# Kernel optimization log

Measured on AMD Instinct MI355X. Metric: run time of the kernel, lower is better.

## Reference

```python
import jax, jax.numpy as jnp
import numpy as np

C = 512
GROUPS = 8
EPS = 1e-5


def setup_inputs() -> dict:
    key = jax.random.key(0)
    ks = jax.random.split(key, 7)
    B, H, W = 16, 32, 32
    x = jax.random.normal(ks[0], (B, C, H, W), dtype=jnp.float32)
    # GroupNorm affine params
    gn_scale = jnp.ones((C,), jnp.float32)
    gn_bias = jnp.zeros((C,), jnp.float32)
    # 1x1 convs == channel matmuls
    s_qkv = 1.0 / np.sqrt(C)
    qkv_w = jax.random.uniform(ks[1], (3 * C, C), jnp.float32, -s_qkv, s_qkv)
    qkv_b = jax.random.uniform(ks[2], (3 * C,), jnp.float32, -s_qkv, s_qkv)
    proj_w = jax.random.uniform(ks[3], (C, C), jnp.float32, -s_qkv, s_qkv)
    proj_b = jax.random.uniform(ks[4], (C,), jnp.float32, -s_qkv, s_qkv)
    return {"x": x, "gn_scale": gn_scale, "gn_bias": gn_bias,
            "qkv_w": qkv_w, "qkv_b": qkv_b, "proj_w": proj_w, "proj_b": proj_b}


def _group_norm(x, scale, bias):
    B, c, H, W = x.shape
    xg = x.reshape(B, GROUPS, c // GROUPS, H, W)
    mean = xg.mean(axis=(2, 3, 4), keepdims=True)
    var = xg.var(axis=(2, 3, 4), keepdims=True)
    xn = ((xg - mean) * jax.lax.rsqrt(var + EPS)).reshape(B, c, H, W)
    return xn * scale[None, :, None, None] + bias[None, :, None, None]


def reference(x, gn_scale, gn_bias, qkv_w, qkv_b, proj_w, proj_b):
    B, c, H, W = x.shape
    N = H * W
    h = _group_norm(x, gn_scale, gn_bias)            # [B,C,H,W]
    hf = h.reshape(B, c, N)                          # flatten spatial
    qkv = jnp.einsum('oc,bcn->bon', qkv_w, hf) + qkv_b[None, :, None]  # [B,3C,N]
    q, k, v = jnp.split(qkv, 3, axis=1)              # each [B,C,N]
    attn = jnp.einsum('bci,bcj->bij', q, k) * (c ** -0.5)  # [B,N,N]
    attn = jax.nn.softmax(attn, axis=2)
    out = jnp.einsum('bij,bcj->bci', attn, v)        # [B,C,N]
    out = jnp.einsum('oc,bcn->bon', proj_w, out) + proj_b[None, :, None]
    return out.reshape(B, c, H, W) + x
```

## Files before the change

kernel.cpp:

```cpp
#include <hip/hip_runtime.h>

typedef __bf16 bf16x8 __attribute__((ext_vector_type(8)));
typedef float f32x4 __attribute__((ext_vector_type(4)));
typedef unsigned short u16;

__device__ __forceinline__ u16 f2bf(float f) {
  unsigned u = __float_as_uint(f);
  u += 0x7fffu + ((u >> 16) & 1u);
  return (u16)(u >> 16);
}
__device__ __forceinline__ float bf2f(u16 h) {
  return __uint_as_float(((unsigned)h) << 16);
}

#define GLOAD_LDS(g, l)                                              \
  __builtin_amdgcn_global_load_lds(                                  \
      (const __attribute__((address_space(1))) void*)(g),            \
      (__attribute__((address_space(3))) void*)(l), 16, 0, 0)

template <int K>
__device__ __forceinline__ void gemm_core_s(const u16* __restrict__ Ab,
                                            const u16* __restrict__ Bb,
                                            f32x4 acc[4][4]) {
  __shared__ __align__(16) u16 As[2][8192], Bs[2][8192];
  const int tid = threadIdx.x;
  const int wave = tid >> 6, lane = tid & 63;
  const int sr = tid >> 3;
  const int sc = ((tid ^ sr) & 7) << 3;
  const u16* ag = Ab + (size_t)sr * K + sc;
  const u16* bg = Bb + (size_t)sr * K + sc;
  const int ldst = tid * 8;
  const int wr = (wave >> 1) << 6, wc = (wave & 1) << 6;
  const int lrow = lane & 15, klane = lane >> 4;
  const int rx = lrow & 7;
  const int ao = (wr + lrow) * 64 + ((klane ^ rx) << 3);
  const int bo = (wc + lrow) * 64 + ((klane ^ rx) << 3);

  const u16 *a_cur = As[0] + ldst, *a_nxt = As[1] + ldst;
  const u16 *b_cur = Bs[0] + ldst, *b_nxt = Bs[1] + ldst;
  const u16 *ar = As[0], *br = Bs[0];
  const u16 *an = As[1], *bn = Bs[1];

#pragma unroll
  for (int r = 0; r < 4; r++) GLOAD_LDS(ag + (size_t)(r * 32) * K, a_cur + r * 2048);
#pragma unroll
  for (int r = 0; r < 4; r++) GLOAD_LDS(bg + (size_t)(r * 32) * K, b_cur + r * 2048);
  __syncthreads();

  for (int k = 64; k < K; k += 64) {
#pragma unroll
    for (int r = 0; r < 4; r++) GLOAD_LDS(ag + (size_t)(r * 32) * K + k, a_nxt + r * 2048);
#pragma unroll
    for (int r = 0; r < 4; r++) GLOAD_LDS(bg + (size_t)(r * 32) * K + k, b_nxt + r * 2048);
#pragma unroll
    for (int half = 0; half < 2; half++) {
      const int xo = half << 5;
      bf16x8 a[4], b[4];
#pragma unroll
      for (int i = 0; i < 4; i++) a[i] = *(const bf16x8*)(ar + ((ao ^ xo) + (i << 10)));
#pragma unroll
      for (int i = 0; i < 4; i++) b[i] = *(const bf16x8*)(br + ((bo ^ xo) + (i << 10)));
#pragma unroll
      for (int mi = 0; mi < 4; mi++)
#pragma unroll
        for (int ni = 0; ni < 4; ni++)
          acc[mi][ni] = __builtin_amdgcn_mfma_f32_16x16x32_bf16(a[mi], b[ni], acc[mi][ni], 0, 0, 0);
    }
    __syncthreads();
    const u16* t;
    t = a_cur; a_cur = a_nxt; a_nxt = t;
    t = b_cur; b_cur = b_nxt; b_nxt = t;
    t = ar; ar = an; an = t;
    t = br; br = bn; bn = t;
  }
#pragma unroll
  for (int half = 0; half < 2; half++) {
    const int xo = half << 5;
    bf16x8 a[4], b[4];
#pragma unroll
    for (int i = 0; i < 4; i++) a[i] = *(const bf16x8*)(ar + ((ao ^ xo) + (i << 10)));
#pragma unroll
    for (int i = 0; i < 4; i++) b[i] = *(const bf16x8*)(br + ((bo ^ xo) + (i << 10)));
#pragma unroll
    for (int mi = 0; mi < 4; mi++)
#pragma unroll
      for (int ni = 0; ni < 4; ni++)
        acc[mi][ni] = __builtin_amdgcn_mfma_f32_16x16x32_bf16(a[mi], b[ni], acc[mi][ni], 0, 0, 0);
  }
}

#define ACC_INIT                                     \
  f32x4 acc[4][4];                                   \
  {                                                  \
    const f32x4 _z = {0.f, 0.f, 0.f, 0.f};           \
    _Pragma("unroll")                                \
    for (int _i = 0; _i < 4; _i++)                   \
      _Pragma("unroll")                              \
      for (int _j = 0; _j < 4; _j++) acc[_i][_j] = _z; \
  }

#define EPI_SETUP                                                            \
  const int tid = threadIdx.x;                                               \
  const int wave = tid >> 6;                                                 \
  const int lane = tid & 63;                                                 \
  const int mb = (blockIdx.y << 7) + ((wave >> 1) << 6) + (((lane >> 4) & 3) << 2); \
  const int nb = (blockIdx.x << 7) + ((wave & 1) << 6) + (lane & 15);

__global__ void __launch_bounds__(256) k_convw(const float* __restrict__ qw,
                                               const float* __restrict__ pw,
                                               u16* __restrict__ wq, u16* __restrict__ wp) {
  const int t = blockIdx.x * 256 + threadIdx.x;
  for (int i = t; i < 786432; i += 262144) wq[i] = f2bf(qw[i]);
  wp[t] = f2bf(pw[t]);
}

__global__ void __launch_bounds__(256) k_gn1(const float* __restrict__ x,
                                             float* __restrict__ part) {
  const int blk = blockIdx.x;
  const float4* src = (const float4*)(x + ((size_t)(blk >> 2) * 64 + (blk & 3) * 16) * 1024);
  float s1 = 0.f, s2 = 0.f;
  for (int i = threadIdx.x; i < 4096; i += 256) {
    float4 v = src[i];
    s1 += v.x + v.y + v.z + v.w;
    s2 += v.x * v.x + v.y * v.y + v.z * v.z + v.w * v.w;
  }
#pragma unroll
  for (int off = 32; off; off >>= 1) { s1 += __shfl_xor(s1, off); s2 += __shfl_xor(s2, off); }
  __shared__ float red[8];
  const int wave = threadIdx.x >> 6, lane = threadIdx.x & 63;
  if (lane == 0) { red[wave] = s1; red[4 + wave] = s2; }
  __syncthreads();
  if (threadIdx.x == 0) {
    part[blk * 2]     = red[0] + red[1] + red[2] + red[3];
    part[blk * 2 + 1] = red[4] + red[5] + red[6] + red[7];
  }
}

__global__ void __launch_bounds__(128) k_gn1b(const float* __restrict__ part,
                                              float* __restrict__ stats) {
  const int g = threadIdx.x;
  const float s1 = part[g * 8 + 0] + part[g * 8 + 2] + part[g * 8 + 4] + part[g * 8 + 6];
  const float s2 = part[g * 8 + 1] + part[g * 8 + 3] + part[g * 8 + 5] + part[g * 8 + 7];
  const float mean = s1 * (1.f / 65536.f);
  const float var = s2 * (1.f / 65536.f) - mean * mean;
  stats[g * 2]     = mean;
  stats[g * 2 + 1] = rsqrtf(var + 1e-5f);
}

__global__ void __launch_bounds__(256) k_gn2(const float* __restrict__ x,
                                             const float* __restrict__ gsc,
                                             const float* __restrict__ gbi,
                                             const float* __restrict__ stats,
                                             u16* __restrict__ h) {
  const int chunk = blockIdx.x & 7, g = (blockIdx.x >> 3) & 7, b = blockIdx.x >> 6;
  const int bg = b * 8 + g;
  const float mean = stats[bg * 2], rstd = stats[bg * 2 + 1];
  const float* xb = x + ((size_t)b * 512 + g * 64) * 1024;
  const int tid = threadIdx.x, wave = tid >> 6, lane = tid & 63;
  __shared__ u16 tile[64][66];
#pragma unroll
  for (int half = 0; half < 2; half++) {
    const int n0 = chunk * 128 + half * 64;
    if (half) __syncthreads();
#pragma unroll
    for (int r = 0; r < 16; r++) {
      const int cl = (r << 2) + wave;
      const int ch = (g << 6) + cl;
      float v = xb[(size_t)cl * 1024 + n0 + lane];
      tile[lane][cl] = f2bf((v - mean) * rstd * gsc[ch] + gbi[ch]);
    }
    __syncthreads();
#pragma unroll
    for (int r = 0; r < 16; r++) {
      const int nl = (r << 2) + wave;
      h[((size_t)b * 1024 + n0 + nl) * 512 + (g << 6) + lane] = tile[nl][lane];
    }
  }
}

__global__ void __launch_bounds__(256) k_qkv(const u16* __restrict__ W,
                                             const u16* __restrict__ h,
                                             const float* __restrict__ bias,
                                             u16* __restrict__ qt, u16* __restrict__ kt,
                                             u16* __restrict__ vv) {
  const int b = blockIdx.z;
  ACC_INIT
  gemm_core_s<512>(W + ((size_t)blockIdx.y << 7) * 512,
                   h + ((size_t)b << 19) + (((size_t)blockIdx.x << 7) * 512), acc);
  EPI_SETUP
  const int sel = blockIdx.y >> 2;
  const float scale = 0.044194173824159216f;
  if (sel < 2) {
    u16* dst = sel ? kt : qt;
    const float sc = sel ? 1.f : scale;
    const int obase = mb - sel * 512;
#pragma unroll
    for (int mi = 0; mi < 4; mi++) {
      const int o = mb + mi * 16;
#pragma unroll
      for (int ni = 0; ni < 4; ni++) {
        const int n = nb + ni * 16;
        ushort4 pk;
        pk.x = f2bf((acc[mi][ni][0] + bias[o + 0]) * sc);
        pk.y = f2bf((acc[mi][ni][1] + bias[o + 1]) * sc);
        pk.z = f2bf((acc[mi][ni][2] + bias[o + 2]) * sc);
        pk.w = f2bf((acc[mi][ni][3] + bias[o + 3]) * sc);
        *(ushort4*)(dst + ((size_t)b * 1024 + n) * 512 + (obase + mi * 16)) = pk;
      }
    }
  } else {
#pragma unroll
    for (int mi = 0; mi < 4; mi++) {
      const int o = mb + mi * 16;
#pragma unroll
      for (int ni = 0; ni < 4; ni++) {
        const int n = nb + ni * 16;
#pragma unroll
        for (int r = 0; r < 4; r++) {
          float val = acc[mi][ni][r] + bias[o + r];
          vv[((size_t)b * 512 + (o - 1024 + r)) * 1024 + n] = f2bf(val);
        }
      }
    }
  }
}

__global__ void __launch_bounds__(256) k_sgemm(const u16* __restrict__ qt,
                                               const u16* __restrict__ kt,
                                               u16* __restrict__ S) {
  const int b = blockIdx.z;
  ACC_INIT
  gemm_core_s<512>(qt + ((size_t)b << 19) + ((size_t)blockIdx.y << 7) * 512,
                   kt + ((size_t)b << 19) + ((size_t)blockIdx.x << 7) * 512, acc);
  EPI_SETUP
  const size_t base = (size_t)b << 20;
#pragma unroll
  for (int mi = 0; mi < 4; mi++)
#pragma unroll
    for (int ni = 0; ni < 4; ni++) {
      const int j = nb + ni * 16;
#pragma unroll
      for (int r = 0; r < 4; r++)
        S[base + (size_t)(mb + mi * 16 + r) * 1024 + j] = f2bf(acc[mi][ni][r]);
    }
}

__global__ void __launch_bounds__(256) k_softmax(u16* __restrict__ S) {
  const size_t base = (((size_t)blockIdx.y << 10) + blockIdx.x) << 10;
  const int tid = threadIdx.x;
  const int wave = tid >> 6, lane = tid & 63;
  ushort4 raw = *(const ushort4*)(S + base + tid * 4);
  float v0 = bf2f(raw.x), v1 = bf2f(raw.y), v2 = bf2f(raw.z), v3 = bf2f(raw.w);
  float m = fmaxf(fmaxf(v0, v1), fmaxf(v2, v3));
#pragma unroll
  for (int off = 32; off; off >>= 1) m = fmaxf(m, __shfl_xor(m, off));
  __shared__ float s1[4], s2[4];
  if (lane == 0) s1[wave] = m;
  __syncthreads();
  m = fmaxf(fmaxf(s1[0], s1[1]), fmaxf(s1[2], s1[3]));
  v0 = __expf(v0 - m); v1 = __expf(v1 - m); v2 = __expf(v2 - m); v3 = __expf(v3 - m);
  float s = v0 + v1 + v2 + v3;
#pragma unroll
  for (int off = 32; off; off >>= 1) s += __shfl_xor(s, off);
  if (lane == 0) s2[wave] = s;
  __syncthreads();
  s = s2[0] + s2[1] + s2[2] + s2[3];
  const float inv = 1.0f / s;
  raw.x = f2bf(v0 * inv); raw.y = f2bf(v1 * inv);
  raw.z = f2bf(v2 * inv); raw.w = f2bf(v3 * inv);
  *(ushort4*)(S + base + tid * 4) = raw;
}

__global__ void __launch_bounds__(256) k_ogemm(const u16* __restrict__ vv,
                                               const u16* __restrict__ P,
                                               u16* __restrict__ ot) {
  const int b = blockIdx.z;
  ACC_INIT
  gemm_core_s<1024>(vv + ((size_t)b << 19) + ((size_t)blockIdx.y << 7) * 1024,
                    P + ((size_t)b << 20) + ((size_t)blockIdx.x << 7) * 1024, acc);
  EPI_SETUP
#pragma unroll
  for (int mi = 0; mi < 4; mi++) {
    const int c = mb + mi * 16;
#pragma unroll
    for (int ni = 0; ni < 4; ni++) {
      const int i = nb + ni * 16;
      ushort4 pk;
      pk.x = f2bf(acc[mi][ni][0]);
      pk.y = f2bf(acc[mi][ni][1]);
      pk.z = f2bf(acc[mi][ni][2]);
      pk.w = f2bf(acc[mi][ni][3]);
      *(ushort4*)(ot + ((size_t)b << 19) + (size_t)i * 512 + c) = pk;
    }
  }
}

__global__ void __launch_bounds__(256) k_proj(const u16* __restrict__ W,
                                              const u16* __restrict__ ot,
                                              const float* __restrict__ pb,
                                              const float* __restrict__ x,
                                              float* __restrict__ out) {
  const int b = blockIdx.z;
  ACC_INIT
  gemm_core_s<512>(W + ((size_t)blockIdx.y << 7) * 512,
                   ot + ((size_t)b << 19) + ((size_t)blockIdx.x << 7) * 512, acc);
  EPI_SETUP
#pragma unroll
  for (int mi = 0; mi < 4; mi++) {
    const int o = mb + mi * 16;
#pragma unroll
    for (int ni = 0; ni < 4; ni++) {
      const int n = nb + ni * 16;
      const size_t base = ((size_t)b * 512 + o) * 1024 + n;
#pragma unroll
      for (int r = 0; r < 4; r++)
        out[base + (size_t)r * 1024] = acc[mi][ni][r] + pb[o + r] + x[base + (size_t)r * 1024];
    }
  }
}

extern "C" void kernel_launch(void* const* d_in, const int* in_sizes, int n_in,
                              void* d_out, int out_size, void* d_ws, size_t ws_size,
                              hipStream_t stream) {
  const float* x     = (const float*)d_in[0];
  const float* gsc   = (const float*)d_in[1];
  const float* gbi   = (const float*)d_in[2];
  const float* qkvw  = (const float*)d_in[3];
  const float* qkvb  = (const float*)d_in[4];
  const float* projw = (const float*)d_in[5];
  const float* projb = (const float*)d_in[6];
  float* out = (float*)d_out;

  char* ws = (char*)d_ws;
  u16* wq = (u16*)(ws);
  u16* wp = (u16*)(ws + 1572864);
  u16* h  = (u16*)(ws + 2097152);
  u16* qt = (u16*)(ws + 18874368);
  u16* kt = (u16*)(ws + 35651584);
  u16* vv = (u16*)(ws + 52428864);
  u16* S  = (u16*)(ws + 69206080);
  u16* ot = h;
  float* part  = (float*)(ws + 69206080);
  float* stats = (float*)(ws + 69206080 + 8192);

  k_convw<<<1024, 256, 0, stream>>>(qkvw, projw, wq, wp);
  k_gn1<<<512, 256, 0, stream>>>(x, part);
  k_gn1b<<<1, 128, 0, stream>>>(part, stats);
  k_gn2<<<1024, 256, 0, stream>>>(x, gsc, gbi, stats, h);
  k_qkv<<<dim3(8, 12, 16), 256, 0, stream>>>(wq, h, qkvb, qt, kt, vv);
  k_sgemm<<<dim3(8, 8, 16), 256, 0, stream>>>(qt, kt, S);
  k_softmax<<<dim3(1024, 16), 256, 0, stream>>>(S);
  k_ogemm<<<dim3(8, 4, 16), 256, 0, stream>>>(vv, S, ot);
  k_proj<<<dim3(8, 4, 16), 256, 0, stream>>>(wp, ot, projb, x, out);
}
```

Baseline: 250.6 us.

## Swizzle GEMM blocks across XCDs and fuse small GroupNorm/weight-convert kernels

Adds an XCD-aware block index remap to all four GEMM kernels, so that consecutive logical tiles (the same batch and neighbouring tiles) land on the same XCD and share its L2. It also folds the weight bf16 conversion into the GroupNorm statistics kernel and moves the tiny stats-finalize kernel into k_gn2, which removes two launches. The cost is extra integer division in each GEMM block and more work per block in k_gn1.

```diff
diff --git a/kernel.cpp b/kernel.cpp
--- a/kernel.cpp
+++ b/kernel.cpp
@@ -11,6 +11,17 @@
 }
 __device__ __forceinline__ float bf2f(u16 h) {
   return __uint_as_float(((unsigned)h) << 16);
+}
+
+__device__ __forceinline__ int3 xcd_swz(int gx, int gy, int gz) {
+  const int D = blockIdx.x + gx * (blockIdx.y + gy * blockIdx.z);
+  const int cpx = (gx * gy * gz) >> 3;
+  const int L = (D & 7) * cpx + (D >> 3);
+  int3 r;
+  r.x = L % gx;
+  r.y = (L / gx) % gy;
+  r.z = L / (gx * gy);
+  return r;
 }
 
 #define GLOAD_LDS(g, l)                                              \
@@ -99,23 +110,19 @@
       for (int _j = 0; _j < 4; _j++) acc[_i][_j] = _z; \
   }
 
-#define EPI_SETUP                                                            \
+#define EPI_SETUP(BX, BY)                                                    \
   const int tid = threadIdx.x;                                               \
   const int wave = tid >> 6;                                                 \
   const int lane = tid & 63;                                                 \
-  const int mb = (blockIdx.y << 7) + ((wave >> 1) << 6) + (((lane >> 4) & 3) << 2); \
-  const int nb = (blockIdx.x << 7) + ((wave & 1) << 6) + (lane & 15);
-
-__global__ void __launch_bounds__(256) k_convw(const float* __restrict__ qw,
-                                               const float* __restrict__ pw,
-                                               u16* __restrict__ wq, u16* __restrict__ wp) {
-  const int t = blockIdx.x * 256 + threadIdx.x;
-  for (int i = t; i < 786432; i += 262144) wq[i] = f2bf(qw[i]);
-  wp[t] = f2bf(pw[t]);
-}
+  const int mb = ((BY) << 7) + ((wave >> 1) << 6) + (((lane >> 4) & 3) << 2); \
+  const int nb = ((BX) << 7) + ((wave & 1) << 6) + (lane & 15);
 
 __global__ void __launch_bounds__(256) k_gn1(const float* __restrict__ x,
-                                             float* __restrict__ part) {
+                                             const float* __restrict__ qw,
+                                             const float* __restrict__ pw,
+                                             float* __restrict__ part,
+                                             u16* __restrict__ wq,
+                                             u16* __restrict__ wp) {
   const int blk = blockIdx.x;
   const float4* src = (const float4*)(x + ((size_t)(blk >> 2) * 64 + (blk & 3) * 16) * 1024);
   float s1 = 0.f, s2 = 0.f;
@@ -134,27 +141,22 @@
     part[blk * 2]     = red[0] + red[1] + red[2] + red[3];
     part[blk * 2 + 1] = red[4] + red[5] + red[6] + red[7];
   }
-}
-
-__global__ void __launch_bounds__(128) k_gn1b(const float* __restrict__ part,
-                                              float* __restrict__ stats) {
-  const int g = threadIdx.x;
-  const float s1 = part[g * 8 + 0] + part[g * 8 + 2] + part[g * 8 + 4] + part[g * 8 + 6];
-  const float s2 = part[g * 8 + 1] + part[g * 8 + 3] + part[g * 8 + 5] + part[g * 8 + 7];
-  const float mean = s1 * (1.f / 65536.f);
-  const float var = s2 * (1.f / 65536.f) - mean * mean;
-  stats[g * 2]     = mean;
-  stats[g * 2 + 1] = rsqrtf(var + 1e-5f);
+  const int gtid = blk * 256 + threadIdx.x;
+  for (int i = gtid; i < 786432; i += 131072) wq[i] = f2bf(qw[i]);
+  for (int i = gtid; i < 262144; i += 131072) wp[i] = f2bf(pw[i]);
 }
 
 __global__ void __launch_bounds__(256) k_gn2(const float* __restrict__ x,
                                              const float* __restrict__ gsc,
                                              const float* __restrict__ gbi,
-                                             const float* __restrict__ stats,
+                                             const float* __restrict__ part,
                                              u16* __restrict__ h) {
   const int chunk = blockIdx.x & 7, g = (blockIdx.x >> 3) & 7, b = blockIdx.x >> 6;
   const int bg = b * 8 + g;
-  const float mean = stats[bg * 2], rstd = stats[bg * 2 + 1];
+  const float s1 = part[bg * 8 + 0] + part[bg * 8 + 2] + part[bg * 8 + 4] + part[bg * 8 + 6];
+  const float s2 = part[bg * 8 + 1] + part[bg * 8 + 3] + part[bg * 8 + 5] + part[bg * 8 + 7];
+  const float mean = s1 * (1.f / 65536.f);
+  const float rstd = rsqrtf(s2 * (1.f / 65536.f) - mean * mean + 1e-5f);
   const float* xb = x + ((size_t)b * 512 + g * 64) * 1024;
   const int tid = threadIdx.x, wave = tid >> 6, lane = tid & 63;
   __shared__ u16 tile[64][66];
@@ -183,12 +185,13 @@
                                              const float* __restrict__ bias,
                                              u16* __restrict__ qt, u16* __restrict__ kt,
                                              u16* __restrict__ vv) {
-  const int b = blockIdx.z;
+  const int3 bb = xcd_swz(8, 12, 16);
+  const int b = bb.z;
   ACC_INIT
-  gemm_core_s<512>(W + ((size_t)blockIdx.y << 7) * 512,
-                   h + ((size_t)b << 19) + (((size_t)blockIdx.x << 7) * 512), acc);
-  EPI_SETUP
-  const int sel = blockIdx.y >> 2;
+  gemm_core_s<512>(W + ((size_t)bb.y << 7) * 512,
+                   h + ((size_t)b << 19) + (((size_t)bb.x << 7) * 512), acc);
+  EPI_SETUP(bb.x, bb.y)
+  const int sel = bb.y >> 2;
   const float scale = 0.044194173824159216f;
   if (sel < 2) {
     u16* dst = sel ? kt : qt;
@@ -228,11 +231,12 @@
 __global__ void __launch_bounds__(256) k_sgemm(const u16* __restrict__ qt,
                                                const u16* __restrict__ kt,
                                                u16* __restrict__ S) {
-  const int b = blockIdx.z;
+  const int3 bb = xcd_swz(8, 8, 16);
+  const int b = bb.z;
   ACC_INIT
-  gemm_core_s<512>(qt + ((size_t)b << 19) + ((size_t)blockIdx.y << 7) * 512,
-                   kt + ((size_t)b << 19) + ((size_t)blockIdx.x << 7) * 512, acc);
-  EPI_SETUP
+  gemm_core_s<512>(qt + ((size_t)b << 19) + ((size_t)bb.y << 7) * 512,
+                   kt + ((size_t)b << 19) + ((size_t)bb.x << 7) * 512, acc);
+  EPI_SETUP(bb.x, bb.y)
   const size_t base = (size_t)b << 20;
 #pragma unroll
   for (int mi = 0; mi < 4; mi++)
@@ -274,11 +278,12 @@
 __global__ void __launch_bounds__(256) k_ogemm(const u16* __restrict__ vv,
                                                const u16* __restrict__ P,
                                                u16* __restrict__ ot) {
-  const int b = blockIdx.z;
+  const int3 bb = xcd_swz(8, 4, 16);
+  const int b = bb.z;
   ACC_INIT
-  gemm_core_s<1024>(vv + ((size_t)b << 19) + ((size_t)blockIdx.y << 7) * 1024,
-                    P + ((size_t)b << 20) + ((size_t)blockIdx.x << 7) * 1024, acc);
-  EPI_SETUP
+  gemm_core_s<1024>(vv + ((size_t)b << 19) + ((size_t)bb.y << 7) * 1024,
+                    P + ((size_t)b << 20) + ((size_t)bb.x << 7) * 1024, acc);
+  EPI_SETUP(bb.x, bb.y)
 #pragma unroll
   for (int mi = 0; mi < 4; mi++) {
     const int c = mb + mi * 16;
@@ -300,11 +305,12 @@
                                               const float* __restrict__ pb,
                                               const float* __restrict__ x,
                                               float* __restrict__ out) {
-  const int b = blockIdx.z;
+  const int3 bb = xcd_swz(8, 4, 16);
+  const int b = bb.z;
   ACC_INIT
-  gemm_core_s<512>(W + ((size_t)blockIdx.y << 7) * 512,
-                   ot + ((size_t)b << 19) + ((size_t)blockIdx.x << 7) * 512, acc);
-  EPI_SETUP
+  gemm_core_s<512>(W + ((size_t)bb.y << 7) * 512,
+                   ot + ((size_t)b << 19) + ((size_t)bb.x << 7) * 512, acc);
+  EPI_SETUP(bb.x, bb.y)
 #pragma unroll
   for (int mi = 0; mi < 4; mi++) {
     const int o = mb + mi * 16;
@@ -340,13 +346,10 @@
   u16* vv = (u16*)(ws + 52428864);
   u16* S  = (u16*)(ws + 69206080);
   u16* ot = h;
-  float* part  = (float*)(ws + 69206080);
-  float* stats = (float*)(ws + 69206080 + 8192);
-
-  k_convw<<<1024, 256, 0, stream>>>(qkvw, projw, wq, wp);
-  k_gn1<<<512, 256, 0, stream>>>(x, part);
-  k_gn1b<<<1, 128, 0, stream>>>(part, stats);
-  k_gn2<<<1024, 256, 0, stream>>>(x, gsc, gbi, stats, h);
+  float* part = (float*)(ws + 69206080);
+
+  k_gn1<<<512, 256, 0, stream>>>(x, qkvw, projw, part, wq, wp);
+  k_gn2<<<1024, 256, 0, stream>>>(x, gsc, gbi, part, h);
   k_qkv<<<dim3(8, 12, 16), 256, 0, stream>>>(wq, h, qkvb, qt, kt, vv);
   k_sgemm<<<dim3(8, 8, 16), 256, 0, stream>>>(qt, kt, S);
   k_softmax<<<dim3(1024, 16), 256, 0, stream>>>(S);
```

Measured after the change: 235.6 us. -6.0%, faster.
